# Optimization experiments

Hardware: AMD Instinct MI355X
Metric: run time of the kernel (lower is better)

The kernel has to match this reference:

```python
import jax, jax.numpy as jnp
import numpy as np

EMBED_DIM = 1024
VALUE_DIM = 2048
NUM_HEADS = 8
KEY_DIM = EMBED_DIM // NUM_HEADS      # 128
HEAD_DIM = VALUE_DIM // NUM_HEADS     # 256
B, T = 2, 2048
EPS = 1e-6


def _rotate_every_two(x):
    # x: [..., d] with d even; pairs (x0,x1)->(-x1,x0)
    x1 = x[..., ::2]
    x2 = x[..., 1::2]
    return jnp.stack((-x2, x1), axis=-1).reshape(x.shape)


def _theta_shift(x, sin, cos):
    # sin/cos: [T, key_dim] broadcast over [B, H, T, key_dim]
    return x * cos + _rotate_every_two(x) * sin


def setup_inputs() -> dict:
    key = jax.random.key(0)
    ks = jax.random.split(key, 6)
    x = jax.random.normal(ks[0], (B, T, EMBED_DIM), dtype=jnp.float32)

    # rotary angles as in torchscale RetNetRelPos
    angle = 1.0 / (10000.0 ** jnp.linspace(0.0, 1.0, KEY_DIM // 2))
    angle = jnp.repeat(angle, 2)                       # [key_dim], interleaved pairs
    idx = jnp.arange(T, dtype=jnp.float32)
    sin = jnp.sin(idx[:, None] * angle[None, :])       # [T, key_dim]
    cos = jnp.cos(idx[:, None] * angle[None, :])

    # per-head decay mask, normalized by sqrt(row-sum) as in RetNet
    decay = jnp.log(1.0 - 2.0 ** (-5.0 - jnp.arange(NUM_HEADS, dtype=jnp.float32)))
    diff = idx[:, None] - idx[None, :]                 # [T, T]
    exponent = jnp.where(diff >= 0, decay[:, None, None] * diff[None], -jnp.inf)
    mask = jnp.exp(exponent)                           # [H, T, T], lower-triangular decay
    mask = mask / jnp.sqrt(mask.sum(-1, keepdims=True))

    s = 0.02
    Wq = s * jax.random.normal(ks[1], (EMBED_DIM, EMBED_DIM), dtype=jnp.float32)
    Wk = s * jax.random.normal(ks[2], (EMBED_DIM, EMBED_DIM), dtype=jnp.float32)
    Wv = s * jax.random.normal(ks[3], (EMBED_DIM, VALUE_DIM), dtype=jnp.float32)
    Wg = s * jax.random.normal(ks[4], (EMBED_DIM, VALUE_DIM), dtype=jnp.float32)
    Wo = s * jax.random.normal(ks[5], (VALUE_DIM, EMBED_DIM), dtype=jnp.float32)
    return {"x": x, "sin": sin, "cos": cos, "mask": mask,
            "Wq": Wq, "Wk": Wk, "Wv": Wv, "Wg": Wg, "Wo": Wo}


def reference(x, sin, cos, mask, Wq, Wk, Wv, Wg, Wo):
    bsz, tgt_len, _ = x.shape
    scaling = KEY_DIM ** (-0.5)

    q = x @ Wq
    k = (x @ Wk) * scaling
    v = x @ Wv
    g = x @ Wg

    q = q.reshape(bsz, tgt_len, NUM_HEADS, KEY_DIM).transpose(0, 2, 1, 3)  # [B,H,T,kd]
    k = k.reshape(bsz, tgt_len, NUM_HEADS, KEY_DIM).transpose(0, 2, 1, 3)
    qr = _theta_shift(q, sin, cos)
    kr = _theta_shift(k, sin, cos)

    vr = v.reshape(bsz, tgt_len, NUM_HEADS, HEAD_DIM).transpose(0, 2, 1, 3)  # [B,H,T,hd]

    # parallel retention: decay-masked QK^T with abs-sum normalization (detached)
    qk = jnp.einsum('bhtd,bhsd->bhts', qr, kr) * mask[None]
    denom = jnp.clip(jnp.sum(jnp.abs(jax.lax.stop_gradient(qk)), axis=-1, keepdims=True),
                     1.0, 50000.0)
    qk = qk / denom
    out = jnp.einsum('bhts,bhsd->bhtd', qk, vr)          # [B,H,T,hd]
    out = out.transpose(0, 2, 1, 3)                      # [B,T,H,hd]

    # per-head RMSNorm (no affine)
    out = out * jax.lax.rsqrt(jnp.mean(out * out, axis=-1, keepdims=True) + EPS)
    out = out.reshape(bsz, tgt_len, VALUE_DIM)

    out = jax.nn.silu(g) * out
    return out @ Wo
```

## Files before the change

### kernel.cpp

```cpp
#include <hip/hip_runtime.h>
#include <hip/hip_bf16.h>
#include <math.h>

constexpr int T_SEQ = 2048;
constexpr int BB    = 2;
constexpr int EMBED = 1024;
constexpr int VDIM  = 2048;
constexpr int NHEADS = 8;
constexpr int KDIM  = 128;
constexpr int HDIM  = 256;
constexpr int ROWS  = BB * T_SEQ;
constexpr int NALL  = 6144;
constexpr float EPS = 1e-6f;

typedef float  f32x4  __attribute__((ext_vector_type(4)));
typedef __bf16 bf16x8 __attribute__((ext_vector_type(8)));
typedef __bf16 bf16x4 __attribute__((ext_vector_type(4)));

__device__ __forceinline__ void gload16(const void* g, void* l) {
    __builtin_amdgcn_global_load_lds(
        (__attribute__((address_space(1))) void*)g,
        (__attribute__((address_space(3))) void*)l, 16, 0, 0);
}

#define WAITV(n) asm volatile("s_waitcnt vmcnt(" #n ")" ::: "memory")
#define BARRIER() __builtin_amdgcn_s_barrier()

__global__ __launch_bounds__(256)
void prep_all(const float* __restrict__ x, const float* __restrict__ Wq,
              const float* __restrict__ Wk, const float* __restrict__ Wv,
              const float* __restrict__ Wg, const float* __restrict__ Wo,
              __bf16* __restrict__ xb,
              __bf16* __restrict__ WqT, __bf16* __restrict__ WkT,
              __bf16* __restrict__ WvT, __bf16* __restrict__ WgT,
              __bf16* __restrict__ WoT) {
    const int bid = blockIdx.x;
    const int x_ = threadIdx.x, y_ = threadIdx.y;
    if (bid >= 8192) {
        const int i = (bid - 8192) * 256 + y_ * 32 + x_;
        float4 v = reinterpret_cast<const float4*>(x)[i];
        bf16x4 o = { (__bf16)v.x, (__bf16)v.y, (__bf16)v.z, (__bf16)v.w };
        reinterpret_cast<bf16x4*>(xb)[i] = o;
        return;
    }
    const float* W; __bf16* WT; int K, N, cx, cy;
    if (bid < 1024)      { W = Wq; WT = WqT; K = 1024; N = 1024; int rm = bid;        cx = rm & 31; cy = rm >> 5; }
    else if (bid < 2048) { W = Wk; WT = WkT; K = 1024; N = 1024; int rm = bid - 1024; cx = rm & 31; cy = rm >> 5; }
    else if (bid < 4096) { W = Wv; WT = WvT; K = 1024; N = 2048; int rm = bid - 2048; cx = rm & 63; cy = rm >> 6; }
    else if (bid < 6144) { W = Wg; WT = WgT; K = 1024; N = 2048; int rm = bid - 4096; cx = rm & 63; cy = rm >> 6; }
    else                 { W = Wo; WT = WoT; K = 2048; N = 1024; int rm = bid - 6144; cx = rm & 31; cy = rm >> 5; }

    __shared__ float tile[32][33];
    const int c0 = cx * 32, k0 = cy * 32;
    #pragma unroll
    for (int p = 0; p < 4; ++p)
        tile[y_ + p * 8][x_] = W[(size_t)(k0 + y_ + p * 8) * N + c0 + x_];
    __syncthreads();
    #pragma unroll
    for (int p = 0; p < 4; ++p)
        WT[(size_t)(c0 + y_ + p * 8) * K + k0 + x_] = (__bf16)tile[x_][y_ + p * 8];
}

__global__ __launch_bounds__(256)
void gemm_qkvg(const __bf16* __restrict__ A, const __bf16* __restrict__ BT,
               __bf16* __restrict__ Qb, __bf16* __restrict__ Kb,
               __bf16* __restrict__ Vt, __bf16* __restrict__ Gb,
               const float* __restrict__ sinT, const float* __restrict__ cosT) {
    constexpr int K = EMBED;
    __shared__ __align__(16) char smem[36864];
    __bf16* As = (__bf16*)smem;
    __bf16* Bs = (__bf16*)(smem + 16384);

    const int bid = blockIdx.x;
    const int swzb = (bid & 7) * 192 + (bid >> 3);
    const int rowBase = (swzb / 48) * 128;
    const int colBase = (swzb % 48) * 128;

    const int tid = threadIdx.x;
    const int w = tid >> 6, lane = tid & 63;
    const int g = lane >> 4, r = lane & 15;
    const int wm = w >> 1, wn = w & 1;

    const int vr  = lane >> 3;
    const int swz = ((lane & 7) ^ vr) * 8;
    const __bf16* aSb = A  + (size_t)(rowBase + 32 * w + vr) * K + swz;
    const __bf16* bSb = BT + (size_t)(colBase + 32 * w + vr) * K + swz;

    f32x4 acc[4][4];
    #pragma unroll
    for (int i = 0; i < 4; ++i)
        #pragma unroll
        for (int j = 0; j < 4; ++j)
            acc[i][j] = (f32x4){0.f, 0.f, 0.f, 0.f};

    for (int k0 = 0; k0 < K; k0 += 64) {
        __syncthreads();
        #pragma unroll
        for (int p = 0; p < 4; ++p) {
            const int cc = 4 * w + p;
            gload16(aSb + (size_t)(8 * p) * K + k0, smem         + cc * 1024);
            gload16(bSb + (size_t)(8 * p) * K + k0, smem + 16384 + cc * 1024);
        }
        __syncthreads();

        #pragma unroll
        for (int kk = 0; kk < 2; ++kk) {
            bf16x8 bfrag[4];
            #pragma unroll
            for (int nf = 0; nf < 4; ++nf) {
                const int row = wn * 64 + nf * 16 + r;
                bfrag[nf] = *reinterpret_cast<const bf16x8*>(
                    &Bs[row * 64 + (((kk << 2) + g) ^ (r & 7)) * 8]);
            }
            #pragma unroll
            for (int mf = 0; mf < 4; ++mf) {
                const int row = wm * 64 + mf * 16 + r;
                bf16x8 a = *reinterpret_cast<const bf16x8*>(
                    &As[row * 64 + (((kk << 2) + g) ^ (r & 7)) * 8]);
                #pragma unroll
                for (int nf = 0; nf < 4; ++nf)
                    acc[mf][nf] = __builtin_amdgcn_mfma_f32_16x16x32_bf16(a, bfrag[nf], acc[mf][nf], 0, 0, 0);
            }
        }
    }

    constexpr float kscale = 0.08838834764831845f;
    if (colBase >= 2048 && colBase < 4096) {
        __syncthreads();
        __bf16* Es = (__bf16*)smem + w * (64 * 72);
        #pragma unroll
        for (int mf = 0; mf < 4; ++mf)
            #pragma unroll
            for (int nf = 0; nf < 4; ++nf) {
                bf16x4 v = { (__bf16)acc[mf][nf][0], (__bf16)acc[mf][nf][1],
                             (__bf16)acc[mf][nf][2], (__bf16)acc[mf][nf][3] };
                *reinterpret_cast<bf16x4*>(&Es[(nf * 16 + r) * 72 + mf * 16 + g * 4]) = v;
            }
        __syncthreads();
        const int t0g = rowBase + wm * 64;
        const int bq = t0g >> 11, tl = t0g & 2047;
        const int colV0 = (colBase - 2048) + wn * 64;
        const int h = colV0 >> 8, dd0 = colV0 & 255;
        const int li = lane & 7, rgrp = lane >> 3;
        __bf16* vtb = Vt + ((size_t)(bq * NHEADS + h) * HDIM + dd0) * T_SEQ + tl;
        #pragma unroll
        for (int c = 0; c < 8; ++c) {
            const int drow = 8 * c + rgrp;
            bf16x8 v = *reinterpret_cast<const bf16x8*>(&Es[drow * 72 + li * 8]);
            *reinterpret_cast<bf16x8*>(vtb + (size_t)drow * T_SEQ + li * 8) = v;
        }
        return;
    }

    __bf16* dst; int dstride, cofs; float alphaSeg; bool rot;
    if (colBase < 1024)      { dst = Qb; dstride = 1024; cofs = colBase;        alphaSeg = 1.0f;   rot = true;  }
    else if (colBase < 2048) { dst = Kb; dstride = 1024; cofs = colBase - 1024; alphaSeg = kscale; rot = true;  }
    else                     { dst = Gb; dstride = 2048; cofs = colBase - 4096; alphaSeg = 1.0f;   rot = false; }

    #pragma unroll
    for (int mf = 0; mf < 4; ++mf)
        #pragma unroll
        for (int nf = 0; nf < 4; ++nf)
            #pragma unroll
            for (int j = 0; j < 4; ++j) {
                const int row  = rowBase + wm * 64 + mf * 16 + g * 4 + j;
                const int colL = cofs + wn * 64 + nf * 16 + r;
                float v = acc[mf][nf][j] * alphaSeg;
                if (rot) {
                    const float p = __shfl_xor(v, 1);
                    const int t  = row & (T_SEQ - 1);
                    const int dh = colL & (KDIM - 1);
                    const float c = cosT[t * KDIM + dh];
                    const float s = sinT[t * KDIM + dh];
                    v = (r & 1) ? (v * c + p * s) : (v * c - p * s);
                }
                dst[(size_t)row * dstride + colL] = (__bf16)v;
            }
}

__global__ __launch_bounds__(256)
void gemm_wo(const __bf16* __restrict__ A, const __bf16* __restrict__ BT,
             float* __restrict__ C) {
    constexpr int N = EMBED, K = VDIM;
    __shared__ __align__(16) char smem[24576];
    __bf16* As = (__bf16*)smem;
    __bf16* Bs = (__bf16*)(smem + 8192);

    const int bid = blockIdx.x;
    const int swzb = (bid & 7) * 64 + (bid >> 3);
    const int rowBase = (swzb >> 3) * 64;
    const int colBase = (swzb & 7) * 128;

    const int tid = threadIdx.x;
    const int w = tid >> 6, lane = tid & 63;
    const int g = lane >> 4, r = lane & 15;
    const int wm = w >> 1, wn = w & 1;

    const int vr  = lane >> 3;
    const int swz = ((lane & 7) ^ vr) * 8;
    const __bf16* aSb = A  + (size_t)(rowBase + 16 * w + vr) * K + swz;
    const __bf16* bSb = BT + (size_t)(colBase + 32 * w + vr) * K + swz;

    f32x4 acc[2][4];
    #pragma unroll
    for (int i = 0; i < 2; ++i)
        #pragma unroll
        for (int j = 0; j < 4; ++j)
            acc[i][j] = (f32x4){0.f, 0.f, 0.f, 0.f};

    for (int k0 = 0; k0 < K; k0 += 64) {
        __syncthreads();
        #pragma unroll
        for (int p = 0; p < 2; ++p) {
            const int cc = 2 * w + p;
            gload16(aSb + (size_t)(8 * p) * K + k0, smem + cc * 1024);
        }
        #pragma unroll
        for (int p = 0; p < 4; ++p) {
            const int cc = 4 * w + p;
            gload16(bSb + (size_t)(8 * p) * K + k0, smem + 8192 + cc * 1024);
        }
        __syncthreads();

        #pragma unroll
        for (int kk = 0; kk < 2; ++kk) {
            bf16x8 bfrag[4];
            #pragma unroll
            for (int nf = 0; nf < 4; ++nf) {
                const int row = wn * 64 + nf * 16 + r;
                bfrag[nf] = *reinterpret_cast<const bf16x8*>(
                    &Bs[row * 64 + (((kk << 2) + g) ^ (r & 7)) * 8]);
            }
            #pragma unroll
            for (int mf = 0; mf < 2; ++mf) {
                const int row = wm * 32 + mf * 16 + r;
                bf16x8 a = *reinterpret_cast<const bf16x8*>(
                    &As[row * 64 + (((kk << 2) + g) ^ (r & 7)) * 8]);
                #pragma unroll
                for (int nf = 0; nf < 4; ++nf)
                    acc[mf][nf] = __builtin_amdgcn_mfma_f32_16x16x32_bf16(a, bfrag[nf], acc[mf][nf], 0, 0, 0);
            }
        }
    }

    #pragma unroll
    for (int mf = 0; mf < 2; ++mf)
        #pragma unroll
        for (int nf = 0; nf < 4; ++nf)
            #pragma unroll
            for (int j = 0; j < 4; ++j) {
                const int row = rowBase + wm * 32 + mf * 16 + g * 4 + j;
                const int col = colBase + wn * 64 + nf * 16 + r;
                C[(size_t)row * N + col] = acc[mf][nf][j];
            }
}

__global__ __launch_bounds__(256)
void retention_mfma(const __bf16* __restrict__ Qb, const __bf16* __restrict__ Kb,
                    const __bf16* __restrict__ Vt,
                    const __bf16* __restrict__ Gb, __bf16* __restrict__ Yb) {
    const int tid = threadIdx.x;
    const int w = tid >> 6, lane = tid & 63;
    const int g = lane >> 4, r = lane & 15;
    const int rx = r & 7;
    const int bid = blockIdx.x;
    const int h = bid & 7;
    const int slot = bid >> 3;
    const int b = slot & 1;
    const int x = slot >> 1;
    const int qt = (b == 0) ? (31 - x) : x;
    const int tt0 = qt * 64;
    const int trow0 = w * 16;

    __shared__ __align__(16) __bf16 Ks[2][64][128];
    __shared__ __align__(16) __bf16 Vs[256][64];
    __shared__ __align__(16) __bf16 Ps[4][16][72];

    const float rho   = 1.0f - exp2f(-(float)(5 + h));
    const float l2r   = log2f(rho);
    const float inv1m = exp2f((float)(5 + h));
    int   tj[4];
    float nrm[4];
    #pragma unroll
    for (int j = 0; j < 4; ++j) {
        tj[j] = tt0 + trow0 + g * 4 + j;
        nrm[j] = rsqrtf((1.0f - exp2f(l2r * (float)(tj[j] + 1))) * inv1m);
    }
    float pneg[4];
    #pragma unroll
    for (int ssub = 0; ssub < 4; ++ssub)
        pneg[ssub] = exp2f(-l2r * (float)(ssub * 16 + r));

    bf16x8 qf[4];
    {
        const __bf16* qrow = Qb + ((size_t)(b * T_SEQ + tt0 + trow0 + r)) * EMBED + h * KDIM;
        #pragma unroll
        for (int kb = 0; kb < 4; ++kb)
            qf[kb] = *reinterpret_cast<const bf16x8*>(qrow + kb * 32 + g * 8);
    }

    f32x4 acc[16];
    #pragma unroll
    for (int db = 0; db < 16; ++db) acc[db] = (f32x4){0.f, 0.f, 0.f, 0.f};
    float dsum[4] = {0.f, 0.f, 0.f, 0.f};

    const __bf16* vtbase = Vt + ((size_t)(b * NHEADS + h) * HDIM) * T_SEQ;
    const __bf16* kbase  = Kb + ((size_t)(b * T_SEQ)) * EMBED + h * KDIM;

    const int klr = lane >> 4;
    const int kc  = lane & 15;
    const int kswz_even = (kc ^ klr) * 8;
    const int kswz_odd  = (kc ^ (4 + klr)) * 8;
    const int vlr  = lane >> 3;
    const int vswz = ((lane & 7) ^ vlr) * 8;

    #pragma unroll
    for (int p = 0; p < 4; ++p) {
        const int cc = 4 * w + p;
        const int se = (p & 1) ? kswz_odd : kswz_even;
        gload16(kbase + (size_t)(4 * cc + klr) * EMBED + se,
                (char*)&Ks[0][0][0] + cc * 1024);
    }

    int cur = 0;
    const int nS = qt + 1;
    for (int st = 0; st < nS; ++st) {
        const int ss0 = st * 64;
        WAITV(0);
        BARRIER();

        #pragma unroll
        for (int p = 0; p < 8; ++p) {
            const int cc = 8 * w + p;
            gload16(vtbase + (size_t)(8 * cc + vlr) * T_SEQ + ss0 + vswz,
                    (char*)&Vs[0][0] + cc * 1024);
        }
        const bool more = (st + 1 < nS);
        if (more) {
            const int ssn = ss0 + 64;
            #pragma unroll
            for (int p = 0; p < 4; ++p) {
                const int cc = 4 * w + p;
                const int se = (p & 1) ? kswz_odd : kswz_even;
                gload16(kbase + (size_t)(ssn + 4 * cc + klr) * EMBED + se,
                        (char*)&Ks[cur ^ 1][0][0] + cc * 1024);
            }
        }

        float wj[4];
        #pragma unroll
        for (int j = 0; j < 4; ++j)
            wj[j] = exp2f(l2r * (float)(tj[j] - ss0)) * nrm[j];
        const bool diag = (st == qt);

        #pragma unroll
        for (int ssub = 0; ssub < 4; ++ssub) {
            f32x4 sacc = (f32x4){0.f, 0.f, 0.f, 0.f};
            #pragma unroll
            for (int kb = 0; kb < 4; ++kb) {
                bf16x8 kf = *reinterpret_cast<const bf16x8*>(
                    &Ks[cur][ssub * 16 + r][((kb * 4 + g) ^ rx) * 8]);
                sacc = __builtin_amdgcn_mfma_f32_16x16x32_bf16(qf[kb], kf, sacc, 0, 0, 0);
            }
            const int scol = ss0 + ssub * 16 + r;
            const float mfac = pneg[ssub];
            #pragma unroll
            for (int j = 0; j < 4; ++j) {
                float pv = sacc[j] * (wj[j] * mfac);
                if (diag && scol > tj[j]) pv = 0.f;
                dsum[j] += fabsf(pv);
                Ps[w][g * 4 + j][ssub * 16 + r] = (__bf16)pv;
            }
        }

        if (more) { WAITV(4); }
        else      { WAITV(0); }
        BARRIER();

        #pragma unroll
        for (int sh = 0; sh < 2; ++sh) {
            bf16x8 pf = *reinterpret_cast<const bf16x8*>(&Ps[w][r][sh * 32 + g * 8]);
            #pragma unroll
            for (int db = 0; db < 16; ++db) {
                bf16x8 vf = *reinterpret_cast<const bf16x8*>(
                    &Vs[db * 16 + r][((sh * 4 + g) ^ rx) * 8]);
                acc[db] = __builtin_amdgcn_mfma_f32_16x16x32_bf16(pf, vf, acc[db], 0, 0, 0);
            }
        }
        cur ^= 1;
    }

    #pragma unroll
    for (int j = 0; j < 4; ++j) {
        float v = dsum[j];
        v += __shfl_xor(v, 1); v += __shfl_xor(v, 2);
        v += __shfl_xor(v, 4); v += __shfl_xor(v, 8);
        dsum[j] = fminf(fmaxf(v, 1.0f), 50000.0f);
    }
    float ss[4] = {0.f, 0.f, 0.f, 0.f};
    #pragma unroll
    for (int db = 0; db < 16; ++db)
        #pragma unroll
        for (int j = 0; j < 4; ++j) {
            const float v = acc[db][j] / dsum[j];
            acc[db][j] = v;
            ss[j] = fmaf(v, v, ss[j]);
        }
    #pragma unroll
    for (int j = 0; j < 4; ++j) {
        float v = ss[j];
        v += __shfl_xor(v, 1); v += __shfl_xor(v, 2);
        v += __shfl_xor(v, 4); v += __shfl_xor(v, 8);
        ss[j] = rsqrtf(v * (1.0f / 256.0f) + EPS);
    }
    #pragma unroll
    for (int j = 0; j < 4; ++j) {
        const size_t row = (size_t)(b * T_SEQ + tj[j]);
        const __bf16* grow = Gb + row * VDIM + h * HDIM;
        __bf16* yrow = Yb + row * VDIM + h * HDIM;
        #pragma unroll
        for (int db = 0; db < 16; ++db) {
            const int c = db * 16 + r;
            const float gv = (float)grow[c];
            const float sil = gv / (1.0f + expf(-gv));
            yrow[c] = (__bf16)(sil * acc[db][j] * ss[j]);
        }
    }
}

extern "C" void kernel_launch(void* const* d_in, const int* in_sizes, int n_in,
                              void* d_out, int out_size, void* d_ws, size_t ws_size,
                              hipStream_t stream) {
    (void)in_sizes; (void)n_in; (void)out_size; (void)ws_size;

    const float* x    = (const float*)d_in[0];
    const float* sinT = (const float*)d_in[1];
    const float* cosT = (const float*)d_in[2];
    const float* Wq   = (const float*)d_in[4];
    const float* Wk   = (const float*)d_in[5];
    const float* Wv   = (const float*)d_in[6];
    const float* Wg   = (const float*)d_in[7];
    const float* Wo   = (const float*)d_in[8];
    float* out = (float*)d_out;

    char* wsp = (char*)d_ws;
    __bf16* xb  = (__bf16*)(wsp);
    __bf16* WqT = (__bf16*)(wsp + (8u  << 20));
    __bf16* WkT = (__bf16*)(wsp + (10u << 20));
    __bf16* WvT = (__bf16*)(wsp + (12u << 20));
    __bf16* WgT = (__bf16*)(wsp + (16u << 20));
    __bf16* WoT = (__bf16*)(wsp + (20u << 20));
    __bf16* Qb  = (__bf16*)(wsp + (24u << 20));
    __bf16* Kb  = (__bf16*)(wsp + (32u << 20));
    __bf16* Yb  = (__bf16*)(wsp + (40u << 20));
    __bf16* Gb  = (__bf16*)(wsp + (56u << 20));
    __bf16* Vt  = (__bf16*)(wsp + (72u << 20));
    __bf16* WTall = WqT;

    const dim3 blk(256);
    const dim3 tblk(32, 8);

    prep_all<<<12288, tblk, 0, stream>>>(x, Wq, Wk, Wv, Wg, Wo,
                                         xb, WqT, WkT, WvT, WgT, WoT);

    gemm_qkvg<<<1536, blk, 0, stream>>>(xb, WTall, Qb, Kb, Vt, Gb, sinT, cosT);

    retention_mfma<<<512, blk, 0, stream>>>(Qb, Kb, Vt, Gb, Yb);

    gemm_wo<<<512, blk, 0, stream>>>(Yb, WoT, out);
}
```

Baseline: 191.5 us.

## Rewrite QKVG GEMM as 256x256 tiles with 8 waves and double-buffered LDS pipeline

The fused Q/K/V/G projection GEMM moves from 128x128 tiles with 4 waves and single-buffered synchronous loads to 256x256 tiles with 8 waves, launched as 384 blocks of 512 threads. It uses a 128KB double-buffered LDS ring where the next K-slice is loaded asynchronously in quarter steps interleaved with MFMA phases, with s_setprio raising priority during the MFMA bursts. The goal is more data reuse per LDS byte and hiding global-load latency behind compute. In exchange, each block holds far more LDS and registers, with 32 accumulators per thread. Only 384 blocks exist, which may leave CUs unevenly loaded, and the V-transpose epilogue now runs in two halves.

Result: slower. 223.6 us (+16.8%).

```diff
diff --git a/kernel.cpp b/kernel.cpp
--- a/kernel.cpp
+++ b/kernel.cpp
@@ -10,7 +10,6 @@
 constexpr int KDIM  = 128;
 constexpr int HDIM  = 256;
 constexpr int ROWS  = BB * T_SEQ;
-constexpr int NALL  = 6144;
 constexpr float EPS = 1e-6f;
 
 typedef float  f32x4  __attribute__((ext_vector_type(4)));
@@ -61,109 +60,135 @@
         WT[(size_t)(c0 + y_ + p * 8) * K + k0 + x_] = (__bf16)tile[x_][y_ + p * 8];
 }
 
-__global__ __launch_bounds__(256)
+#define STAGEH(ISB, TAU, HF) do { \
+    const __bf16* s_ = ((ISB) ? BT : A) + \
+        (size_t)((((ISB) ? colBase : rowBase)) + (HF) * 128 + w * 8 + srow) * 1024 + \
+        (TAU) * 64 + swz; \
+    char* d_ = smem + ((ISB) ? 65536 : 0) + (((TAU) & 1) * 2 + (HF)) * 16384 + w * 1024; \
+    gload16(s_, d_); \
+    gload16(s_ + (size_t)64 * 1024, d_ + 8192); \
+} while (0)
+
+#define QPHASE(TAU, Q, STGSTMT) do { \
+    const int p_ = (TAU) & 1; \
+    const __bf16* Ab_ = (const __bf16*)(smem + (p_ * 2 + wm) * 16384); \
+    const __bf16* Bb_ = (const __bf16*)(smem + 65536 + (p_ * 2 + bh) * 16384); \
+    if ((Q) == 0) { \
+        _Pragma("unroll") for (int nf = 0; nf < 4; ++nf) \
+        _Pragma("unroll") for (int kk = 0; kk < 2; ++kk) \
+            bq[nf][kk] = *(const bf16x8*)(Bb_ + (bro + nf * 16) * 64 + ((kk * 4 + g) ^ rx) * 8); \
+    } \
+    bf16x8 aq_[2][2]; \
+    _Pragma("unroll") for (int i = 0; i < 2; ++i) \
+    _Pragma("unroll") for (int kk = 0; kk < 2; ++kk) \
+        aq_[i][kk] = *(const bf16x8*)(Ab_ + (((Q) * 2 + i) * 16 + r) * 64 + ((kk * 4 + g) ^ rx) * 8); \
+    STGSTMT; \
+    BARRIER(); \
+    __builtin_amdgcn_s_setprio(1); \
+    _Pragma("unroll") for (int i = 0; i < 2; ++i) \
+    _Pragma("unroll") for (int nf = 0; nf < 4; ++nf) \
+    _Pragma("unroll") for (int kk = 0; kk < 2; ++kk) \
+        acc[(Q) * 2 + i][nf] = __builtin_amdgcn_mfma_f32_16x16x32_bf16( \
+            aq_[i][kk], bq[nf][kk], acc[(Q) * 2 + i][nf], 0, 0, 0); \
+    __builtin_amdgcn_s_setprio(0); \
+} while (0)
+
+__global__ __launch_bounds__(512, 2)
 void gemm_qkvg(const __bf16* __restrict__ A, const __bf16* __restrict__ BT,
                __bf16* __restrict__ Qb, __bf16* __restrict__ Kb,
                __bf16* __restrict__ Vt, __bf16* __restrict__ Gb,
                const float* __restrict__ sinT, const float* __restrict__ cosT) {
-    constexpr int K = EMBED;
-    __shared__ __align__(16) char smem[36864];
-    __bf16* As = (__bf16*)smem;
-    __bf16* Bs = (__bf16*)(smem + 16384);
+    __shared__ __align__(16) char smem[131072];
 
     const int bid = blockIdx.x;
-    const int swzb = (bid & 7) * 192 + (bid >> 3);
-    const int rowBase = (swzb / 48) * 128;
-    const int colBase = (swzb % 48) * 128;
+    const int bx = (bid & 7) * 3 + ((bid >> 3) % 3);
+    const int by = (bid >> 3) / 3;
+    const int rowBase = by * 256;
+    const int colBase = bx * 256;
 
     const int tid = threadIdx.x;
     const int w = tid >> 6, lane = tid & 63;
     const int g = lane >> 4, r = lane & 15;
-    const int wm = w >> 1, wn = w & 1;
-
-    const int vr  = lane >> 3;
-    const int swz = ((lane & 7) ^ vr) * 8;
-    const __bf16* aSb = A  + (size_t)(rowBase + 32 * w + vr) * K + swz;
-    const __bf16* bSb = BT + (size_t)(colBase + 32 * w + vr) * K + swz;
-
-    f32x4 acc[4][4];
-    #pragma unroll
-    for (int i = 0; i < 4; ++i)
+    const int wm = w >> 2, wn = w & 3;
+    const int rx = r & 7;
+    const int bh = wn >> 1;
+    const int bro = (wn & 1) * 64 + r;
+
+    const int srow = lane >> 3;
+    const int swz  = ((lane & 7) ^ srow) * 8;
+
+    f32x4 acc[8][4];
+    #pragma unroll
+    for (int i = 0; i < 8; ++i)
         #pragma unroll
         for (int j = 0; j < 4; ++j)
             acc[i][j] = (f32x4){0.f, 0.f, 0.f, 0.f};
-
-    for (int k0 = 0; k0 < K; k0 += 64) {
-        __syncthreads();
-        #pragma unroll
-        for (int p = 0; p < 4; ++p) {
-            const int cc = 4 * w + p;
-            gload16(aSb + (size_t)(8 * p) * K + k0, smem         + cc * 1024);
-            gload16(bSb + (size_t)(8 * p) * K + k0, smem + 16384 + cc * 1024);
-        }
-        __syncthreads();
-
-        #pragma unroll
-        for (int kk = 0; kk < 2; ++kk) {
-            bf16x8 bfrag[4];
-            #pragma unroll
-            for (int nf = 0; nf < 4; ++nf) {
-                const int row = wn * 64 + nf * 16 + r;
-                bfrag[nf] = *reinterpret_cast<const bf16x8*>(
-                    &Bs[row * 64 + (((kk << 2) + g) ^ (r & 7)) * 8]);
-            }
-            #pragma unroll
-            for (int mf = 0; mf < 4; ++mf) {
-                const int row = wm * 64 + mf * 16 + r;
-                bf16x8 a = *reinterpret_cast<const bf16x8*>(
-                    &As[row * 64 + (((kk << 2) + g) ^ (r & 7)) * 8]);
-                #pragma unroll
-                for (int nf = 0; nf < 4; ++nf)
-                    acc[mf][nf] = __builtin_amdgcn_mfma_f32_16x16x32_bf16(a, bfrag[nf], acc[mf][nf], 0, 0, 0);
-            }
-        }
+    bf16x8 bq[4][2];
+
+    STAGEH(1, 0, 0); STAGEH(1, 0, 1);
+    STAGEH(0, 0, 0); STAGEH(0, 0, 1);
+    STAGEH(1, 1, 0); STAGEH(1, 1, 1);
+    WAITV(4);
+    BARRIER();
+
+    for (int it = 0; it < 8; ++it) {
+        const int e = 2 * it, o = e + 1;
+        const bool more = (it < 7);
+        QPHASE(e, 0, STAGEH(0, o, 0));                        BARRIER();
+        QPHASE(e, 1, STAGEH(0, o, 1));                        BARRIER();
+        QPHASE(e, 2, if (more) STAGEH(1, e + 2, 0));          BARRIER();
+        QPHASE(e, 3, if (more) STAGEH(1, e + 2, 1));
+        if (more) { WAITV(4); } else { WAITV(0); }            BARRIER();
+        QPHASE(o, 0, if (more) STAGEH(0, e + 2, 0));          BARRIER();
+        QPHASE(o, 1, if (more) STAGEH(0, e + 2, 1));          BARRIER();
+        QPHASE(o, 2, if (more) STAGEH(1, o + 2, 0));          BARRIER();
+        QPHASE(o, 3, if (more) STAGEH(1, o + 2, 1));
+        if (more) { WAITV(4); } else { WAITV(0); }            BARRIER();
     }
 
     constexpr float kscale = 0.08838834764831845f;
-    if (colBase >= 2048 && colBase < 4096) {
-        __syncthreads();
-        __bf16* Es = (__bf16*)smem + w * (64 * 72);
-        #pragma unroll
-        for (int mf = 0; mf < 4; ++mf)
-            #pragma unroll
-            for (int nf = 0; nf < 4; ++nf) {
-                bf16x4 v = { (__bf16)acc[mf][nf][0], (__bf16)acc[mf][nf][1],
-                             (__bf16)acc[mf][nf][2], (__bf16)acc[mf][nf][3] };
-                *reinterpret_cast<bf16x4*>(&Es[(nf * 16 + r) * 72 + mf * 16 + g * 4]) = v;
-            }
-        __syncthreads();
-        const int t0g = rowBase + wm * 64;
-        const int bq = t0g >> 11, tl = t0g & 2047;
+    if (bx >= 8 && bx < 16) {
+        __bf16* Es = (__bf16*)smem + w * 4608;
         const int colV0 = (colBase - 2048) + wn * 64;
         const int h = colV0 >> 8, dd0 = colV0 & 255;
         const int li = lane & 7, rgrp = lane >> 3;
-        __bf16* vtb = Vt + ((size_t)(bq * NHEADS + h) * HDIM + dd0) * T_SEQ + tl;
-        #pragma unroll
-        for (int c = 0; c < 8; ++c) {
-            const int drow = 8 * c + rgrp;
-            bf16x8 v = *reinterpret_cast<const bf16x8*>(&Es[drow * 72 + li * 8]);
-            *reinterpret_cast<bf16x8*>(vtb + (size_t)drow * T_SEQ + li * 8) = v;
+        #pragma unroll
+        for (int h2 = 0; h2 < 2; ++h2) {
+            #pragma unroll
+            for (int mf = 0; mf < 4; ++mf)
+                #pragma unroll
+                for (int nf = 0; nf < 4; ++nf) {
+                    f32x4 a = acc[h2 * 4 + mf][nf];
+                    bf16x4 v = { (__bf16)a[0], (__bf16)a[1], (__bf16)a[2], (__bf16)a[3] };
+                    *reinterpret_cast<bf16x4*>(&Es[(nf * 16 + r) * 72 + mf * 16 + g * 4]) = v;
+                }
+            __syncthreads();
+            const int t0g = rowBase + wm * 128 + h2 * 64;
+            const int bq_ = t0g >> 11, tl = t0g & 2047;
+            __bf16* vtb = Vt + ((size_t)(bq_ * NHEADS + h) * HDIM + dd0) * T_SEQ + tl;
+            #pragma unroll
+            for (int c = 0; c < 8; ++c) {
+                const int drow = 8 * c + rgrp;
+                bf16x8 v = *reinterpret_cast<const bf16x8*>(&Es[drow * 72 + li * 8]);
+                *reinterpret_cast<bf16x8*>(vtb + (size_t)drow * T_SEQ + li * 8) = v;
+            }
+            __syncthreads();
         }
         return;
     }
 
     __bf16* dst; int dstride, cofs; float alphaSeg; bool rot;
-    if (colBase < 1024)      { dst = Qb; dstride = 1024; cofs = colBase;        alphaSeg = 1.0f;   rot = true;  }
-    else if (colBase < 2048) { dst = Kb; dstride = 1024; cofs = colBase - 1024; alphaSeg = kscale; rot = true;  }
-    else                     { dst = Gb; dstride = 2048; cofs = colBase - 4096; alphaSeg = 1.0f;   rot = false; }
-
-    #pragma unroll
-    for (int mf = 0; mf < 4; ++mf)
+    if (bx < 4)       { dst = Qb; dstride = 1024; cofs = colBase;        alphaSeg = 1.0f;   rot = true;  }
+    else if (bx < 8)  { dst = Kb; dstride = 1024; cofs = colBase - 1024; alphaSeg = kscale; rot = true;  }
+    else              { dst = Gb; dstride = 2048; cofs = colBase - 4096; alphaSeg = 1.0f;   rot = false; }
+
+    #pragma unroll
+    for (int mf = 0; mf < 8; ++mf)
         #pragma unroll
         for (int nf = 0; nf < 4; ++nf)
             #pragma unroll
             for (int j = 0; j < 4; ++j) {
-                const int row  = rowBase + wm * 64 + mf * 16 + g * 4 + j;
+                const int row  = rowBase + wm * 128 + mf * 16 + g * 4 + j;
                 const int colL = cofs + wn * 64 + nf * 16 + r;
                 float v = acc[mf][nf][j] * alphaSeg;
                 if (rot) {
@@ -373,8 +398,7 @@
             }
         }
 
-        if (more) { WAITV(4); }
-        else      { WAITV(0); }
+        if (more) { WAITV(4); } else { WAITV(0); }
         BARRIER();
 
         #pragma unroll
@@ -463,7 +487,7 @@
     prep_all<<<12288, tblk, 0, stream>>>(x, Wq, Wk, Wv, Wg, Wo,
                                          xb, WqT, WkT, WvT, WgT, WoT);
 
-    gemm_qkvg<<<1536, blk, 0, stream>>>(xb, WTall, Qb, Kb, Vt, Gb, sinT, cosT);
+    gemm_qkvg<<<384, 512, 0, stream>>>(xb, WTall, Qb, Kb, Vt, Gb, sinT, cosT);
 
     retention_mfma<<<512, blk, 0, stream>>>(Qb, Kb, Vt, Gb, Yb);
 
```
